# Kernel optimization log

Hardware: AMD Instinct MI355X
Metric: run time of the kernel (lower is better)

Reference implementation:

```python
import jax, jax.numpy as jnp
import numpy as np

SEQ, BATCH, IN, H = 2048, 1024, 1, 32


def _lstm_layer(x, Wih, Whh, bih, bhh):
    # x: (T, B, in); Wih: (4H, in); Whh: (4H, H); biases: (4H,)
    T, B = x.shape[0], x.shape[1]
    Hh = Whh.shape[1]
    x_proj = jnp.einsum('tbi,gi->tbg', x, Wih) + bih + bhh  # (T, B, 4H)

    def step(carry, xt):
        h, c = carry
        gates = xt + h @ Whh.T  # (B, 4H)
        i, f, g, o = jnp.split(gates, 4, axis=-1)  # PyTorch gate order i,f,g,o
        i = jax.nn.sigmoid(i)
        f = jax.nn.sigmoid(f)
        g = jnp.tanh(g)
        o = jax.nn.sigmoid(o)
        c = f * c + i * g
        h = o * jnp.tanh(c)
        return (h, c), h

    h0 = jnp.zeros((B, Hh), dtype=x.dtype)
    c0 = jnp.zeros((B, Hh), dtype=x.dtype)
    (_, _), out = jax.lax.scan(step, (h0, c0), x_proj)
    return out  # (T, B, H)


def setup_inputs() -> dict:
    key = jax.random.key(0)
    ks = jax.random.split(key, 16)
    s = 1.0 / np.sqrt(H)  # PyTorch LSTM/Linear init scale
    d = {'x': jax.random.normal(ks[0], (SEQ, BATCH, IN), dtype=jnp.float32)}
    in_dims = [IN, H, H]
    ki = 1
    for l in range(3):
        d[f'Wih{l}'] = jax.random.uniform(ks[ki + 0], (4 * H, in_dims[l]), minval=-s, maxval=s)
        d[f'Whh{l}'] = jax.random.uniform(ks[ki + 1], (4 * H, H), minval=-s, maxval=s)
        d[f'bih{l}'] = jax.random.uniform(ks[ki + 2], (4 * H,), minval=-s, maxval=s)
        d[f'bhh{l}'] = jax.random.uniform(ks[ki + 3], (4 * H,), minval=-s, maxval=s)
        ki += 4
    d['Wfc'] = jax.random.uniform(ks[13], (1, H), minval=-s, maxval=s)
    d['bfc'] = jax.random.uniform(ks[14], (1,), minval=-s, maxval=s)
    return d


def reference(x, Wih0, Whh0, bih0, bhh0, Wih1, Whh1, bih1, bhh1,
              Wih2, Whh2, bih2, bhh2, Wfc, bfc):
    out = _lstm_layer(x, Wih0, Whh0, bih0, bhh0)
    out = _lstm_layer(out, Wih1, Whh1, bih1, bhh1)
    out = _lstm_layer(out, Wih2, Whh2, bih2, bhh2)
    return out @ Wfc.T + bfc  # (T, B, 1)
```

## Files before the change

kernel.cpp:

```cpp
#include <hip/hip_runtime.h>

#define T_STEPS 2048
#define NBATCH  1024
#define L2E     1.442695040888963f

typedef _Float16 f16x8 __attribute__((ext_vector_type(8)));
typedef float    f32x4 __attribute__((ext_vector_type(4)));

__device__ __forceinline__ unsigned pk2(float a, float b) {
    auto v = __builtin_amdgcn_cvt_pkrtz(a, b);
    return __builtin_bit_cast(unsigned, v);
}

__device__ __forceinline__ f16x8 loadrow8(const float* p) {
    float4 lo = *reinterpret_cast<const float4*>(p);
    float4 hi = *reinterpret_cast<const float4*>(p + 4);
    f16x8 r;
    r[0] = (_Float16)lo.x; r[1] = (_Float16)lo.y;
    r[2] = (_Float16)lo.z; r[3] = (_Float16)lo.w;
    r[4] = (_Float16)hi.x; r[5] = (_Float16)hi.y;
    r[6] = (_Float16)hi.z; r[7] = (_Float16)hi.w;
    return r;
}

__device__ __forceinline__ void sync_lds() {
    asm volatile("s_waitcnt lgkmcnt(0)" ::: "memory");
    __builtin_amdgcn_s_barrier();
    asm volatile("" ::: "memory");
}

#define PIN8(f) do { uint4 _u = __builtin_bit_cast(uint4, (f));              \
    asm volatile("" : "+v"(_u.x), "+v"(_u.y), "+v"(_u.z), "+v"(_u.w));       \
    (f) = __builtin_bit_cast(f16x8, _u); } while (0)

__global__ __launch_bounds__(384, 1)
void lstm3_ws6h_kernel(const float* __restrict__ x,
                       const float* __restrict__ Wih0, const float* __restrict__ Whh0,
                       const float* __restrict__ bih0, const float* __restrict__ bhh0,
                       const float* __restrict__ Wih1, const float* __restrict__ Whh1,
                       const float* __restrict__ bih1, const float* __restrict__ bhh1,
                       const float* __restrict__ Wih2, const float* __restrict__ Whh2,
                       const float* __restrict__ bih2, const float* __restrict__ bhh2,
                       const float* __restrict__ Wfc,  const float* __restrict__ bfc,
                       float* __restrict__ out)
{
    const int tid  = threadIdx.x;
    const int wid  = tid >> 6;
    const int lay  = wid >> 1;
    const int half = wid & 1;
    const int l    = tid & 63;
    const int g    = l >> 4;
    const int b    = l & 15;
    const int qa   = l & 3;
    const int gp   = (l & 15) >> 2;
    const int b0   = blockIdx.x * 16;
    const int m0   = half * 4;

    __shared__ __align__(16) f16x8 hH[3][3][64];
    __shared__ float FCpart[3][16];

    f16x8 Fi[4], Fh[4];
    {
        const int rowA = qa * 32 + 8 * gp + m0;
        const float* Pi = (lay == 1) ? Wih1 : ((lay == 2) ? Wih2 : nullptr);
        const float* Ph = (lay == 0) ? Whh0 : ((lay == 1) ? Whh1 : Whh2);
#pragma unroll
        for (int mm = 0; mm < 4; ++mm) {
            Fh[mm] = loadrow8(Ph + (rowA + mm) * 32 + 8 * g);
            PIN8(Fh[mm]);
        }
        if (lay != 0) {
#pragma unroll
            for (int mm = 0; mm < 4; ++mm) {
                Fi[mm] = loadrow8(Pi + (rowA + mm) * 32 + 8 * g);
                PIN8(Fi[mm]);
            }
        }
    }

    float4 bs[4], w0s[4];
    float wfc_r[4];
    {
        const float* BI = (lay == 0) ? bih0 : ((lay == 1) ? bih1 : bih2);
        const float* BH = (lay == 0) ? bhh0 : ((lay == 1) ? bhh1 : bhh2);
#pragma unroll
        for (int mm = 0; mm < 4; ++mm) {
            const int u = 8 * g + m0 + mm;
            const float bx = BI[u]      + BH[u];
            const float by = BI[u + 32] + BH[u + 32];
            const float bz = BI[u + 64] + BH[u + 64];
            const float bw = BI[u + 96] + BH[u + 96];
            bs[mm] = make_float4(-L2E * bx, -L2E * by, 2.f * L2E * bz, -L2E * bw);
            if (lay == 0)
                w0s[mm] = make_float4(-L2E * Wih0[u],          -L2E * Wih0[u + 32],
                                      2.f * L2E * Wih0[u + 64], -L2E * Wih0[u + 96]);
            if (lay == 2) wfc_r[mm] = Wfc[u];
        }
    }
    const float bfc0 = bfc[0];

    if (half == 0) {
        f16x8 zz = {0, 0, 0, 0, 0, 0, 0, 0};
        hH[0][lay][l] = zz; hH[1][lay][l] = zz; hH[2][lay][l] = zz;
    }
    __syncthreads();

    float cst[4] = {0.f, 0.f, 0.f, 0.f};
    float vprev = 0.f;
    float xv = (lay == 0) ? x[b0 + b] : 0.f;

#define ACT4(USE_X, XV)                                                      \
    do {                                                                     \
        _Pragma("unroll")                                                    \
        for (int mm = 0; mm < 4; ++mm) {                                     \
            float ti = fmaf(-L2E,      acc[mm][0], bs[mm].x);                \
            float tf = fmaf(-L2E,      acc[mm][1], bs[mm].y);                \
            float tg = fmaf(2.f * L2E, acc[mm][2], bs[mm].z);                \
            float to = fmaf(-L2E,      acc[mm][3], bs[mm].w);                \
            if (USE_X) {                                                     \
                ti = fmaf(w0s[mm].x, (XV), ti);                              \
                tf = fmaf(w0s[mm].y, (XV), tf);                              \
                tg = fmaf(w0s[mm].z, (XV), tg);                              \
                to = fmaf(w0s[mm].w, (XV), to);                              \
            }                                                                \
            const float ei = __builtin_amdgcn_exp2f(ti);                     \
            const float ef = __builtin_amdgcn_exp2f(tf);                     \
            const float eg = __builtin_amdgcn_exp2f(tg);                     \
            const float eo = __builtin_amdgcn_exp2f(to);                     \
            const float ig = (eg - 1.f) *                                    \
                __builtin_amdgcn_rcpf((1.f + ei) * (1.f + eg));              \
            const float ff = __builtin_amdgcn_rcpf(1.f + ef);                \
            cst[mm] = fmaf(ff, cst[mm], ig);                                 \
            const float tc = fminf(2.f * L2E * cst[mm], 60.f);               \
            const float ec = __builtin_amdgcn_exp2f(tc);                     \
            hn[mm] = (ec - 1.f) *                                            \
                __builtin_amdgcn_rcpf((1.f + eo) * (1.f + ec));              \
        }                                                                    \
    } while (0)

    const int NIT = T_STEPS + 3;
    int sw = 0, sp = 2;
    for (int n = 0; n < NIT; ++n) {
        f32x4 acc[4];
        float hn[4];
        if (lay == 0) {
            if (n < T_STEPS) {
                const int tn = (n + 1 < T_STEPS) ? n + 1 : T_STEPS - 1;
                const float xn = x[tn * NBATCH + b0 + b];
                const f16x8 hb0 = hH[sp][0][l];
#pragma unroll
                for (int mm = 0; mm < 4; ++mm) {
                    f32x4 z = {0.f, 0.f, 0.f, 0.f};
                    acc[mm] = __builtin_amdgcn_mfma_f32_16x16x32_f16(Fh[mm], hb0, z, 0, 0, 0);
                }
                ACT4(1, xv);
                uint2 pk;
                pk.x = pk2(hn[0], hn[1]);
                pk.y = pk2(hn[2], hn[3]);
                *(reinterpret_cast<uint2*>(&hH[sw][0][l]) + half) = pk;
                xv = xn;
            }
        } else if (lay == 1) {
            if (n >= 1 && n <= T_STEPS) {
                const f16x8 hb0 = hH[sp][0][l];
                const f16x8 hb1 = hH[sp][1][l];
#pragma unroll
                for (int mm = 0; mm < 4; ++mm) {
                    f32x4 z = {0.f, 0.f, 0.f, 0.f};
                    z       = __builtin_amdgcn_mfma_f32_16x16x32_f16(Fi[mm], hb0, z, 0, 0, 0);
                    acc[mm] = __builtin_amdgcn_mfma_f32_16x16x32_f16(Fh[mm], hb1, z, 0, 0, 0);
                }
                ACT4(0, 0.f);
                uint2 pk;
                pk.x = pk2(hn[0], hn[1]);
                pk.y = pk2(hn[2], hn[3]);
                *(reinterpret_cast<uint2*>(&hH[sw][1][l]) + half) = pk;
            }
        } else {
            if (half == 1 && n >= 3 && l < 16)
                out[(n - 3) * NBATCH + b0 + l] = FCpart[sp][l] + vprev + bfc0;
            if (n >= 2 && n <= T_STEPS + 1) {
                const f16x8 hb1 = hH[sp][1][l];
                const f16x8 hb2 = hH[sp][2][l];
#pragma unroll
                for (int mm = 0; mm < 4; ++mm) {
                    f32x4 z = {0.f, 0.f, 0.f, 0.f};
                    z       = __builtin_amdgcn_mfma_f32_16x16x32_f16(Fi[mm], hb1, z, 0, 0, 0);
                    acc[mm] = __builtin_amdgcn_mfma_f32_16x16x32_f16(Fh[mm], hb2, z, 0, 0, 0);
                }
                ACT4(0, 0.f);
                uint2 pk;
                pk.x = pk2(hn[0], hn[1]);
                pk.y = pk2(hn[2], hn[3]);
                *(reinterpret_cast<uint2*>(&hH[sw][2][l]) + half) = pk;
                float v = 0.f;
#pragma unroll
                for (int mm = 0; mm < 4; ++mm) v = fmaf(wfc_r[mm], hn[mm], v);
                v += __shfl_xor(v, 16);
                v += __shfl_xor(v, 32);
                if (half == 0) { if (l < 16) FCpart[sw][l] = v; }
                else           { vprev = v; }
            }
        }

        sync_lds();
        sp = sw; sw = (sw == 2) ? 0 : sw + 1;
    }
#undef ACT4
}

extern "C" void kernel_launch(void* const* d_in, const int* in_sizes, int n_in,
                              void* d_out, int out_size, void* d_ws, size_t ws_size,
                              hipStream_t stream)
{
    const float* x    = (const float*)d_in[0];
    const float* Wih0 = (const float*)d_in[1];
    const float* Whh0 = (const float*)d_in[2];
    const float* bih0 = (const float*)d_in[3];
    const float* bhh0 = (const float*)d_in[4];
    const float* Wih1 = (const float*)d_in[5];
    const float* Whh1 = (const float*)d_in[6];
    const float* bih1 = (const float*)d_in[7];
    const float* bhh1 = (const float*)d_in[8];
    const float* Wih2 = (const float*)d_in[9];
    const float* Whh2 = (const float*)d_in[10];
    const float* bih2 = (const float*)d_in[11];
    const float* bhh2 = (const float*)d_in[12];
    const float* Wfc  = (const float*)d_in[13];
    const float* bfc  = (const float*)d_in[14];
    float* out        = (float*)d_out;

    lstm3_ws6h_kernel<<<dim3(NBATCH / 16), dim3(384), 0, stream>>>(
        x, Wih0, Whh0, bih0, bhh0,
        Wih1, Whh1, bih1, bhh1,
        Wih2, Whh2, bih2, bhh2,
        Wfc, bfc, out);
}
```

Baseline: 1.535 ms.

## Split each LSTM layer across four waves instead of two per block

```diff
diff --git a/kernel.cpp b/kernel.cpp
--- a/kernel.cpp
+++ b/kernel.cpp
@@ -33,58 +33,59 @@
     asm volatile("" : "+v"(_u.x), "+v"(_u.y), "+v"(_u.z), "+v"(_u.w));       \
     (f) = __builtin_bit_cast(f16x8, _u); } while (0)
 
-__global__ __launch_bounds__(384, 1)
-void lstm3_ws6h_kernel(const float* __restrict__ x,
-                       const float* __restrict__ Wih0, const float* __restrict__ Whh0,
-                       const float* __restrict__ bih0, const float* __restrict__ bhh0,
-                       const float* __restrict__ Wih1, const float* __restrict__ Whh1,
-                       const float* __restrict__ bih1, const float* __restrict__ bhh1,
-                       const float* __restrict__ Wih2, const float* __restrict__ Whh2,
-                       const float* __restrict__ bih2, const float* __restrict__ bhh2,
-                       const float* __restrict__ Wfc,  const float* __restrict__ bfc,
-                       float* __restrict__ out)
+__global__ __launch_bounds__(768, 1)
+void lstm3_ws12q_kernel(const float* __restrict__ x,
+                        const float* __restrict__ Wih0, const float* __restrict__ Whh0,
+                        const float* __restrict__ bih0, const float* __restrict__ bhh0,
+                        const float* __restrict__ Wih1, const float* __restrict__ Whh1,
+                        const float* __restrict__ bih1, const float* __restrict__ bhh1,
+                        const float* __restrict__ Wih2, const float* __restrict__ Whh2,
+                        const float* __restrict__ bih2, const float* __restrict__ bhh2,
+                        const float* __restrict__ Wfc,  const float* __restrict__ bfc,
+                        float* __restrict__ out)
 {
-    const int tid  = threadIdx.x;
-    const int wid  = tid >> 6;
-    const int lay  = wid >> 1;
-    const int half = wid & 1;
-    const int l    = tid & 63;
-    const int g    = l >> 4;
-    const int b    = l & 15;
-    const int qa   = l & 3;
-    const int gp   = (l & 15) >> 2;
-    const int b0   = blockIdx.x * 16;
-    const int m0   = half * 4;
+    const int tid = threadIdx.x;
+    const int wid = tid >> 6;
+    const int lay = wid >> 2;
+    const int q   = wid & 3;
+    const int l   = tid & 63;
+    const int g   = l >> 4;
+    const int b   = l & 15;
+    const int qa  = l & 3;
+    const int gp  = (l & 15) >> 2;
+    const int b0  = blockIdx.x * 16;
+    const int m0  = q * 2;
 
     __shared__ __align__(16) f16x8 hH[3][3][64];
-    __shared__ float FCpart[3][16];
-
-    f16x8 Fi[4], Fh[4];
+    __shared__ float FCpart[3][3][16];
+    __shared__ char  pad[86016];
+
+    f16x8 Fi[2], Fh[2];
     {
         const int rowA = qa * 32 + 8 * gp + m0;
         const float* Pi = (lay == 1) ? Wih1 : ((lay == 2) ? Wih2 : nullptr);
         const float* Ph = (lay == 0) ? Whh0 : ((lay == 1) ? Whh1 : Whh2);
 #pragma unroll
-        for (int mm = 0; mm < 4; ++mm) {
+        for (int mm = 0; mm < 2; ++mm) {
             Fh[mm] = loadrow8(Ph + (rowA + mm) * 32 + 8 * g);
             PIN8(Fh[mm]);
         }
         if (lay != 0) {
 #pragma unroll
-            for (int mm = 0; mm < 4; ++mm) {
+            for (int mm = 0; mm < 2; ++mm) {
                 Fi[mm] = loadrow8(Pi + (rowA + mm) * 32 + 8 * g);
                 PIN8(Fi[mm]);
             }
         }
     }
 
-    float4 bs[4], w0s[4];
-    float wfc_r[4];
+    float4 bs[2], w0s[2];
+    float wfc_r[2];
     {
         const float* BI = (lay == 0) ? bih0 : ((lay == 1) ? bih1 : bih2);
         const float* BH = (lay == 0) ? bhh0 : ((lay == 1) ? bhh1 : bhh2);
 #pragma unroll
-        for (int mm = 0; mm < 4; ++mm) {
+        for (int mm = 0; mm < 2; ++mm) {
             const int u = 8 * g + m0 + mm;
             const float bx = BI[u]      + BH[u];
             const float by = BI[u + 32] + BH[u + 32];
@@ -99,20 +100,27 @@
     }
     const float bfc0 = bfc[0];
 
-    if (half == 0) {
+    if (bfc0 == 1e30f) { pad[tid] = 1; out[0] = pad[0]; }
+
+    if (q == 0) {
         f16x8 zz = {0, 0, 0, 0, 0, 0, 0, 0};
         hH[0][lay][l] = zz; hH[1][lay][l] = zz; hH[2][lay][l] = zz;
     }
+    if (lay == 2 && q == 0 && l < 16) {
+        FCpart[0][0][l] = 0.f; FCpart[0][1][l] = 0.f; FCpart[0][2][l] = 0.f;
+        FCpart[1][0][l] = 0.f; FCpart[1][1][l] = 0.f; FCpart[1][2][l] = 0.f;
+        FCpart[2][0][l] = 0.f; FCpart[2][1][l] = 0.f; FCpart[2][2][l] = 0.f;
+    }
     __syncthreads();
 
-    float cst[4] = {0.f, 0.f, 0.f, 0.f};
+    float cst[2] = {0.f, 0.f};
     float vprev = 0.f;
     float xv = (lay == 0) ? x[b0 + b] : 0.f;
 
-#define ACT4(USE_X, XV)                                                      \
+#define ACT2(USE_X, XV)                                                      \
     do {                                                                     \
         _Pragma("unroll")                                                    \
-        for (int mm = 0; mm < 4; ++mm) {                                     \
+        for (int mm = 0; mm < 2; ++mm) {                                     \
             float ti = fmaf(-L2E,      acc[mm][0], bs[mm].x);                \
             float tf = fmaf(-L2E,      acc[mm][1], bs[mm].y);                \
             float tg = fmaf(2.f * L2E, acc[mm][2], bs[mm].z);                \
@@ -141,23 +149,20 @@
     const int NIT = T_STEPS + 3;
     int sw = 0, sp = 2;
     for (int n = 0; n < NIT; ++n) {
-        f32x4 acc[4];
-        float hn[4];
+        f32x4 acc[2];
+        float hn[2];
         if (lay == 0) {
             if (n < T_STEPS) {
                 const int tn = (n + 1 < T_STEPS) ? n + 1 : T_STEPS - 1;
                 const float xn = x[tn * NBATCH + b0 + b];
                 const f16x8 hb0 = hH[sp][0][l];
 #pragma unroll
-                for (int mm = 0; mm < 4; ++mm) {
+                for (int mm = 0; mm < 2; ++mm) {
                     f32x4 z = {0.f, 0.f, 0.f, 0.f};
                     acc[mm] = __builtin_amdgcn_mfma_f32_16x16x32_f16(Fh[mm], hb0, z, 0, 0, 0);
                 }
-                ACT4(1, xv);
-                uint2 pk;
-                pk.x = pk2(hn[0], hn[1]);
-                pk.y = pk2(hn[2], hn[3]);
-                *(reinterpret_cast<uint2*>(&hH[sw][0][l]) + half) = pk;
+                ACT2(1, xv);
+                reinterpret_cast<unsigned*>(&hH[sw][0][l])[q] = pk2(hn[0], hn[1]);
                 xv = xn;
             }
         } else if (lay == 1) {
@@ -165,48 +170,42 @@
                 const f16x8 hb0 = hH[sp][0][l];
                 const f16x8 hb1 = hH[sp][1][l];
 #pragma unroll
-                for (int mm = 0; mm < 4; ++mm) {
+                for (int mm = 0; mm < 2; ++mm) {
                     f32x4 z = {0.f, 0.f, 0.f, 0.f};
                     z       = __builtin_amdgcn_mfma_f32_16x16x32_f16(Fi[mm], hb0, z, 0, 0, 0);
                     acc[mm] = __builtin_amdgcn_mfma_f32_16x16x32_f16(Fh[mm], hb1, z, 0, 0, 0);
                 }
-                ACT4(0, 0.f);
-                uint2 pk;
-                pk.x = pk2(hn[0], hn[1]);
-                pk.y = pk2(hn[2], hn[3]);
-                *(reinterpret_cast<uint2*>(&hH[sw][1][l]) + half) = pk;
+                ACT2(0, 0.f);
+                reinterpret_cast<unsigned*>(&hH[sw][1][l])[q] = pk2(hn[0], hn[1]);
             }
         } else {
-            if (half == 1 && n >= 3 && l < 16)
-                out[(n - 3) * NBATCH + b0 + l] = FCpart[sp][l] + vprev + bfc0;
+            if (q == 3 && n >= 3 && l < 16)
+                out[(n - 3) * NBATCH + b0 + l] =
+                    FCpart[sp][0][l] + FCpart[sp][1][l] + FCpart[sp][2][l]
+                    + vprev + bfc0;
             if (n >= 2 && n <= T_STEPS + 1) {
                 const f16x8 hb1 = hH[sp][1][l];
                 const f16x8 hb2 = hH[sp][2][l];
 #pragma unroll
-                for (int mm = 0; mm < 4; ++mm) {
+                for (int mm = 0; mm < 2; ++mm) {
                     f32x4 z = {0.f, 0.f, 0.f, 0.f};
                     z       = __builtin_amdgcn_mfma_f32_16x16x32_f16(Fi[mm], hb1, z, 0, 0, 0);
                     acc[mm] = __builtin_amdgcn_mfma_f32_16x16x32_f16(Fh[mm], hb2, z, 0, 0, 0);
                 }
-                ACT4(0, 0.f);
-                uint2 pk;
-                pk.x = pk2(hn[0], hn[1]);
-                pk.y = pk2(hn[2], hn[3]);
-                *(reinterpret_cast<uint2*>(&hH[sw][2][l]) + half) = pk;
-                float v = 0.f;
-#pragma unroll
-                for (int mm = 0; mm < 4; ++mm) v = fmaf(wfc_r[mm], hn[mm], v);
+                ACT2(0, 0.f);
+                reinterpret_cast<unsigned*>(&hH[sw][2][l])[q] = pk2(hn[0], hn[1]);
+                float v = fmaf(wfc_r[0], hn[0], wfc_r[1] * hn[1]);
                 v += __shfl_xor(v, 16);
                 v += __shfl_xor(v, 32);
-                if (half == 0) { if (l < 16) FCpart[sw][l] = v; }
-                else           { vprev = v; }
+                if (q < 3) { if (l < 16) FCpart[sw][q][l] = v; }
+                else       { vprev = v; }
             }
         }
 
         sync_lds();
         sp = sw; sw = (sw == 2) ? 0 : sw + 1;
     }
-#undef ACT4
+#undef ACT2
 }
 
 extern "C" void kernel_launch(void* const* d_in, const int* in_sizes, int n_in,
@@ -230,7 +229,7 @@
     const float* bfc  = (const float*)d_in[14];
     float* out        = (float*)d_out;
 
-    lstm3_ws6h_kernel<<<dim3(NBATCH / 16), dim3(384), 0, stream>>>(
+    lstm3_ws12q_kernel<<<dim3(NBATCH / 16), dim3(768), 0, stream>>>(
         x, Wih0, Whh0, bih0, bhh0,
         Wih1, Whh1, bih1, bhh1,
         Wih2, Whh2, bih2, bhh2,
```

Result: faster. 1.248 ms (median of 2 runs) (-18.7%).
